# Kernel tuning notes

Measured on AMD Instinct MI355X. Metric: run time of the kernel, lower is better.

## Reference

```python
import jax, jax.numpy as jnp
import numpy as np

N, E, ND, ED, H1, H2 = 50000, 800000, 128, 16, 256, 32
NEG_SLOPE = 0.2


def setup_inputs() -> dict:
    key = jax.random.key(0)
    ks = jax.random.split(key, 12)
    s = lambda k, shape: jax.random.normal(k, shape, jnp.float32) * 0.05
    return dict(
        x=jax.random.normal(ks[0], (N, ND), jnp.float32),
        edge_index=jax.random.randint(ks[1], (2, E), 0, N),
        edge_attr=jax.random.normal(ks[2], (E, ED), jnp.float32),
        Wl1=s(ks[3], (H1, ND)), bl1=jnp.zeros((H1,), jnp.float32),
        Wr1=s(ks[4], (H1, ND)), br1=jnp.zeros((H1,), jnp.float32),
        We1=s(ks[5], (H1, ED)), att1=s(ks[6], (H1,)), bias1=jnp.zeros((H1,), jnp.float32),
        Wl2=s(ks[7], (H2, H1)), bl2=jnp.zeros((H2,), jnp.float32),
        Wr2=s(ks[8], (H2, H1)), br2=jnp.zeros((H2,), jnp.float32),
        We2=s(ks[9], (H2, ED)), att2=s(ks[10], (H2,)), bias2=jnp.zeros((H2,), jnp.float32),
    )


def _gatv2_layer(x, src, dst, ea, Wl, bl, Wr, br, We, att, bias, n):
    # heads=1, concat=True  (PyG GATv2Conv defaults)
    xl = x @ Wl.T + bl                      # [n, C]  source transform
    xr = x @ Wr.T + br                      # [n, C]  target transform
    # per-edge message: x_j + x_i + lin_edge(edge_attr), then LeakyReLU
    m = jax.nn.leaky_relu(xl[src] + xr[dst] + ea @ We.T, NEG_SLOPE)  # [Etot, C]
    logit = m @ att                         # [Etot]
    # segment softmax over destination nodes (numerically stable)
    lmax = jax.ops.segment_max(logit, dst, num_segments=n)
    lmax = jnp.where(jnp.isfinite(lmax), lmax, 0.0)
    a = jnp.exp(logit - lmax[dst])
    denom = jax.ops.segment_sum(a, dst, num_segments=n)
    a = a / denom[dst]                      # self-loops guarantee denom > 0
    # scatter-add of alpha-weighted source features, plus output bias
    return jax.ops.segment_sum(xl[src] * a[:, None], dst, num_segments=n) + bias


def reference(x, edge_index, edge_attr,
              Wl1, bl1, Wr1, br1, We1, att1, bias1,
              Wl2, bl2, Wr2, br2, We2, att2, bias2):
    n = x.shape[0]
    src, dst = edge_index[0], edge_index[1]
    # add_self_loops=True with fill_value='mean': loop attr = mean incoming edge_attr
    deg = jax.ops.segment_sum(jnp.ones_like(dst, jnp.float32), dst, num_segments=n)
    loop_attr = jax.ops.segment_sum(edge_attr, dst, num_segments=n) / jnp.maximum(deg, 1.0)[:, None]
    loop = jnp.arange(n)
    src_f = jnp.concatenate([src, loop])
    dst_f = jnp.concatenate([dst, loop])
    ea = jnp.concatenate([edge_attr, loop_attr], axis=0)
    h = _gatv2_layer(x, src_f, dst_f, ea, Wl1, bl1, Wr1, br1, We1, att1, bias1, n)
    h = _gatv2_layer(h, src_f, dst_f, ea, Wl2, bl2, Wr2, br2, We2, att2, bias2, n)
    return h.mean(axis=0)  # [out_dim]
```

## Files before the change

kernel.cpp:

```cpp
#include <hip/hip_runtime.h>
#include <math.h>

#define N_NODES 50000
#define N_EDGES 800000
#define ND 128
#define ED 16
#define H1 256
#define H2 32
#define NEG_SLOPE 0.2f

typedef _Float16 half2v __attribute__((ext_vector_type(2)));

#if defined(__has_builtin)
#if __has_builtin(__builtin_amdgcn_fdot2)
#define FDOT2(a, b, c) __builtin_amdgcn_fdot2((a), (b), (c), false)
#endif
#endif
#ifndef FDOT2
#define FDOT2(a, b, c) ((float)(a).x * (float)(b).x + (float)(a).y * (float)(b).y + (c))
#endif

__global__ void k_deg(const int* __restrict__ ei, int* __restrict__ counts, int E) {
    int e = blockIdx.x * blockDim.x + threadIdx.x;
    if (e < E) atomicAdd(&counts[ei[E + e]], 1);
}

__global__ void k_scan1(const int* __restrict__ counts, int* __restrict__ partial, int n, int chunk) {
    __shared__ int sh[256];
    int beg = blockIdx.x * chunk, end = min(beg + chunk, n);
    int sum = 0;
    for (int i = beg + threadIdx.x; i < end; i += 256) sum += counts[i] + 1;
    sh[threadIdx.x] = sum;
    __syncthreads();
    for (int off = 128; off; off >>= 1) {
        if (threadIdx.x < off) sh[threadIdx.x] += sh[threadIdx.x + off];
        __syncthreads();
    }
    if (threadIdx.x == 0) partial[blockIdx.x] = sh[0];
}
__global__ void k_scan2(int* __restrict__ partial) {
    __shared__ int sh[256];
    int v = partial[threadIdx.x];
    sh[threadIdx.x] = v;
    __syncthreads();
    for (int off = 1; off < 256; off <<= 1) {
        int t = (threadIdx.x >= off) ? sh[threadIdx.x - off] : 0;
        __syncthreads();
        sh[threadIdx.x] += t;
        __syncthreads();
    }
    partial[threadIdx.x] = sh[threadIdx.x] - v;
}
__global__ void k_scan3(const int* __restrict__ counts, const int* __restrict__ partial,
                        int* __restrict__ rowptr, int n, int chunk) {
    __shared__ int sh[256];
    int beg = blockIdx.x * chunk, end = min(beg + chunk, n);
    int run = partial[blockIdx.x];
    for (int base = beg; base < end; base += 256) {
        int i = base + threadIdx.x;
        int v = (i < end) ? counts[i] + 1 : 0;
        sh[threadIdx.x] = v;
        __syncthreads();
        for (int off = 1; off < 256; off <<= 1) {
            int t = (threadIdx.x >= off) ? sh[threadIdx.x - off] : 0;
            __syncthreads();
            sh[threadIdx.x] += t;
            __syncthreads();
        }
        if (i < end) rowptr[i + 1] = run + sh[threadIdx.x];
        __syncthreads();
        run += sh[255];
        __syncthreads();
    }
    if (blockIdx.x == 0 && threadIdx.x == 0) rowptr[0] = 0;
}

__global__ void k_fill_csr(const int* __restrict__ ei, const float* __restrict__ ea,
                           const int* __restrict__ rowptr, int* __restrict__ fill,
                           int* __restrict__ csr_src, _Float16* __restrict__ ea_h, int E, int n) {
    int idx = blockIdx.x * blockDim.x + threadIdx.x;
    if (idx < E) {
        int dst = ei[E + idx];
        int slot = rowptr[dst] + atomicAdd(&fill[dst], 1);
        csr_src[slot] = ei[idx];
        const float* srow = ea + (size_t)idx * ED;
        _Float16* drow = ea_h + (size_t)slot * ED;
        #pragma unroll
        for (int q = 0; q < 4; ++q) {
            float4 f = ((const float4*)srow)[q];
            drow[q * 4 + 0] = (_Float16)f.x;
            drow[q * 4 + 1] = (_Float16)f.y;
            drow[q * 4 + 2] = (_Float16)f.z;
            drow[q * 4 + 3] = (_Float16)f.w;
        }
    } else if (idx < E + n) {
        int i = idx - E;
        csr_src[rowptr[i + 1] - 1] = i;
    }
}

__global__ void k_loop_mean(_Float16* __restrict__ ea_h, const int* __restrict__ rowptr, int n) {
    int idx = blockIdx.x * blockDim.x + threadIdx.x;
    if (idx >= n * ED) return;
    int node = idx >> 4, d = idx & 15;
    int beg = rowptr[node], last = rowptr[node + 1] - 1;
    float s = 0.f;
    for (int j = beg; j < last; ++j) s += (float)ea_h[(size_t)j * ED + d];
    int cnt = last - beg;
    ea_h[(size_t)last * ED + d] = (_Float16)(s / (float)(cnt > 0 ? cnt : 1));
}

__global__ void k_pack_half(const float* __restrict__ src, _Float16* __restrict__ dst, int total) {
    int i = blockIdx.x * blockDim.x + threadIdx.x;
    if (i < total) dst[i] = (_Float16)src[i];
}

#define GT 64
#define GK 32
#define LDP 68
__global__ __launch_bounds__(256) void k_gemm_dual(const float* __restrict__ X,
                                                   const float* __restrict__ Wa,
                                                   const float* __restrict__ ba,
                                                   float* __restrict__ Ya,
                                                   const float* __restrict__ Wb,
                                                   const float* __restrict__ bb,
                                                   float* __restrict__ Yb,
                                                   int n, int K, int C) {
    __shared__ float xs[GK][LDP];
    __shared__ float ws[GK][LDP];
    int tid = threadIdx.x;
    int tx = tid & 15, ty = tid >> 4;
    int row0 = blockIdx.x * GT, col0 = blockIdx.y * GT;
    float acc[4][4] = {};
    for (int k0 = 0; k0 < K; k0 += GK) {
        #pragma unroll
        for (int l = 0; l < 2; ++l) {
            int t = l * 256 + tid;
            int r = t >> 3, c4 = t & 7;
            int gr = row0 + r;
            float4 xv = {0.f, 0.f, 0.f, 0.f};
            if (gr < n) xv = *(const float4*)(X + (size_t)gr * K + k0 + c4 * 4);
            xs[c4 * 4 + 0][r] = xv.x; xs[c4 * 4 + 1][r] = xv.y;
            xs[c4 * 4 + 2][r] = xv.z; xs[c4 * 4 + 3][r] = xv.w;
            int gc = col0 + r;
            const float* wrow = (gc < C) ? Wa + (size_t)gc * K : Wb + (size_t)(gc - C) * K;
            float4 wv = *(const float4*)(wrow + k0 + c4 * 4);
            ws[c4 * 4 + 0][r] = wv.x; ws[c4 * 4 + 1][r] = wv.y;
            ws[c4 * 4 + 2][r] = wv.z; ws[c4 * 4 + 3][r] = wv.w;
        }
        __syncthreads();
        #pragma unroll
        for (int kk = 0; kk < GK; ++kk) {
            float4 a = *(const float4*)&xs[kk][ty * 4];
            float4 b = *(const float4*)&ws[kk][tx * 4];
            const float* af = (const float*)&a;
            const float* bf = (const float*)&b;
            #pragma unroll
            for (int i = 0; i < 4; ++i)
                #pragma unroll
                for (int j = 0; j < 4; ++j) acc[i][j] += af[i] * bf[j];
        }
        __syncthreads();
    }
    #pragma unroll
    for (int i = 0; i < 4; ++i) {
        int r = row0 + ty * 4 + i;
        if (r >= n) continue;
        #pragma unroll
        for (int j = 0; j < 4; ++j) {
            int c = col0 + tx * 4 + j;
            if (c < C) Ya[(size_t)r * C + c] = acc[i][j] + ba[c];
            else       Yb[(size_t)r * C + (c - C)] = acc[i][j] + bb[c - C];
        }
    }
}

__global__ __launch_bounds__(256) void k_gat1(const float* __restrict__ xl,
                                              const float* __restrict__ xr,
                                              const _Float16* __restrict__ ea_h,
                                              const _Float16* __restrict__ We_h,
                                              const float* __restrict__ att,
                                              const float* __restrict__ bias,
                                              const int* __restrict__ rowptr,
                                              const int* __restrict__ csr_src,
                                              float* __restrict__ out, int n) {
    int lane = threadIdx.x & 63;
    int wave = (blockIdx.x * blockDim.x + threadIdx.x) >> 6;
    int nwaves = (gridDim.x * blockDim.x) >> 6;
    const half2v* Wp = (const half2v*)We_h;
    half2v w[4][8];
    #pragma unroll
    for (int r = 0; r < 4; ++r)
        #pragma unroll
        for (int q = 0; q < 8; ++q) w[r][q] = Wp[(lane * 4 + r) * 8 + q];
    float4 attv = ((const float4*)att)[lane];
    float4 bv = ((const float4*)bias)[lane];

    for (int node = wave; node < n; node += nwaves) {
        float4 xrv = *(const float4*)(xr + (size_t)node * H1 + lane * 4);
        int beg = rowptr[node], end = rowptr[node + 1];
        float denom = 0.f;
        float4 acc = {0.f, 0.f, 0.f, 0.f};
        int j = beg;
        for (; j + 1 < end; j += 2) {
            int sA = csr_src[j], sB = csr_src[j + 1];
            const half2v* eA = (const half2v*)(ea_h + (size_t)j * ED);
            const half2v* eB = (const half2v*)(ea_h + (size_t)(j + 1) * ED);
            half2v a0 = eA[0], a1 = eA[1], a2 = eA[2], a3 = eA[3];
            half2v a4 = eA[4], a5 = eA[5], a6 = eA[6], a7 = eA[7];
            half2v b0 = eB[0], b1 = eB[1], b2 = eB[2], b3 = eB[3];
            half2v b4 = eB[4], b5 = eB[5], b6 = eB[6], b7 = eB[7];
            float4 xlA = *(const float4*)(xl + (size_t)sA * H1 + lane * 4);
            float4 xlB = *(const float4*)(xl + (size_t)sB * H1 + lane * 4);
            float pA = 0.f, pB = 0.f;
            #pragma unroll
            for (int r = 0; r < 4; ++r) {
                float weA = 0.f, weB = 0.f;
                weA = FDOT2(w[r][0], a0, weA); weB = FDOT2(w[r][0], b0, weB);
                weA = FDOT2(w[r][1], a1, weA); weB = FDOT2(w[r][1], b1, weB);
                weA = FDOT2(w[r][2], a2, weA); weB = FDOT2(w[r][2], b2, weB);
                weA = FDOT2(w[r][3], a3, weA); weB = FDOT2(w[r][3], b3, weB);
                weA = FDOT2(w[r][4], a4, weA); weB = FDOT2(w[r][4], b4, weB);
                weA = FDOT2(w[r][5], a5, weA); weB = FDOT2(w[r][5], b5, weB);
                weA = FDOT2(w[r][6], a6, weA); weB = FDOT2(w[r][6], b6, weB);
                weA = FDOT2(w[r][7], a7, weA); weB = FDOT2(w[r][7], b7, weB);
                float tA = ((const float*)&xlA)[r] + ((const float*)&xrv)[r] + weA;
                float tB = ((const float*)&xlB)[r] + ((const float*)&xrv)[r] + weB;
                tA = (tA > 0.f) ? tA : NEG_SLOPE * tA;
                tB = (tB > 0.f) ? tB : NEG_SLOPE * tB;
                pA += ((const float*)&attv)[r] * tA;
                pB += ((const float*)&attv)[r] * tB;
            }
            #pragma unroll
            for (int off = 32; off >= 1; off >>= 1) {
                pA += __shfl_xor(pA, off);
                pB += __shfl_xor(pB, off);
            }
            float peA = __expf(pA), peB = __expf(pB);
            denom += peA + peB;
            acc.x += peA * xlA.x + peB * xlB.x;
            acc.y += peA * xlA.y + peB * xlB.y;
            acc.z += peA * xlA.z + peB * xlB.z;
            acc.w += peA * xlA.w + peB * xlB.w;
        }
        if (j < end) {
            int sA = csr_src[j];
            const half2v* eA = (const half2v*)(ea_h + (size_t)j * ED);
            half2v a0 = eA[0], a1 = eA[1], a2 = eA[2], a3 = eA[3];
            half2v a4 = eA[4], a5 = eA[5], a6 = eA[6], a7 = eA[7];
            float4 xlA = *(const float4*)(xl + (size_t)sA * H1 + lane * 4);
            float pA = 0.f;
            #pragma unroll
            for (int r = 0; r < 4; ++r) {
                float weA = 0.f;
                weA = FDOT2(w[r][0], a0, weA);
                weA = FDOT2(w[r][1], a1, weA);
                weA = FDOT2(w[r][2], a2, weA);
                weA = FDOT2(w[r][3], a3, weA);
                weA = FDOT2(w[r][4], a4, weA);
                weA = FDOT2(w[r][5], a5, weA);
                weA = FDOT2(w[r][6], a6, weA);
                weA = FDOT2(w[r][7], a7, weA);
                float tA = ((const float*)&xlA)[r] + ((const float*)&xrv)[r] + weA;
                tA = (tA > 0.f) ? tA : NEG_SLOPE * tA;
                pA += ((const float*)&attv)[r] * tA;
            }
            #pragma unroll
            for (int off = 32; off >= 1; off >>= 1) pA += __shfl_xor(pA, off);
            float peA = __expf(pA);
            denom += peA;
            acc.x += peA * xlA.x; acc.y += peA * xlA.y;
            acc.z += peA * xlA.z; acc.w += peA * xlA.w;
        }
        float inv = 1.f / denom;
        float4 o;
        o.x = acc.x * inv + bv.x; o.y = acc.y * inv + bv.y;
        o.z = acc.z * inv + bv.z; o.w = acc.w * inv + bv.w;
        *(float4*)(out + (size_t)node * H1 + lane * 4) = o;
    }
}

__global__ __launch_bounds__(256) void k_gat2(const float* __restrict__ xl,
                                              const float* __restrict__ xr,
                                              const _Float16* __restrict__ ea_h,
                                              const _Float16* __restrict__ We_h,
                                              const float* __restrict__ att,
                                              const float* __restrict__ bias,
                                              const int* __restrict__ rowptr,
                                              const int* __restrict__ csr_src,
                                              float* __restrict__ out, int n) {
    int tid = threadIdx.x;
    int c = tid & 31;
    int grp = (blockIdx.x * blockDim.x + tid) >> 5;
    int ngrp = (gridDim.x * blockDim.x) >> 5;
    const half2v* Wp = (const half2v*)We_h;
    half2v w0 = Wp[c * 8 + 0], w1 = Wp[c * 8 + 1], w2 = Wp[c * 8 + 2], w3 = Wp[c * 8 + 3];
    half2v w4 = Wp[c * 8 + 4], w5 = Wp[c * 8 + 5], w6 = Wp[c * 8 + 6], w7 = Wp[c * 8 + 7];
    float attc = att[c], bc = bias[c];

    for (int node = grp; node < n; node += ngrp) {
        float xrc = xr[(size_t)node * H2 + c];
        int beg = rowptr[node], end = rowptr[node + 1];
        float denom = 0.f, acc = 0.f;
        int j = beg;
        for (; j + 1 < end; j += 2) {
            int sA = csr_src[j], sB = csr_src[j + 1];
            const half2v* eA = (const half2v*)(ea_h + (size_t)j * ED);
            const half2v* eB = (const half2v*)(ea_h + (size_t)(j + 1) * ED);
            half2v a0 = eA[0], a1 = eA[1], a2 = eA[2], a3 = eA[3];
            half2v a4 = eA[4], a5 = eA[5], a6 = eA[6], a7 = eA[7];
            half2v b0 = eB[0], b1 = eB[1], b2 = eB[2], b3 = eB[3];
            half2v b4 = eB[4], b5 = eB[5], b6 = eB[6], b7 = eB[7];
            float xlA = xl[(size_t)sA * H2 + c];
            float xlB = xl[(size_t)sB * H2 + c];
            float weA = 0.f, weB = 0.f;
            weA = FDOT2(w0, a0, weA); weB = FDOT2(w0, b0, weB);
            weA = FDOT2(w1, a1, weA); weB = FDOT2(w1, b1, weB);
            weA = FDOT2(w2, a2, weA); weB = FDOT2(w2, b2, weB);
            weA = FDOT2(w3, a3, weA); weB = FDOT2(w3, b3, weB);
            weA = FDOT2(w4, a4, weA); weB = FDOT2(w4, b4, weB);
            weA = FDOT2(w5, a5, weA); weB = FDOT2(w5, b5, weB);
            weA = FDOT2(w6, a6, weA); weB = FDOT2(w6, b6, weB);
            weA = FDOT2(w7, a7, weA); weB = FDOT2(w7, b7, weB);
            float tA = xlA + xrc + weA;
            float tB = xlB + xrc + weB;
            tA = (tA > 0.f) ? tA : NEG_SLOPE * tA;
            tB = (tB > 0.f) ? tB : NEG_SLOPE * tB;
            float pA = attc * tA, pB = attc * tB;
            #pragma unroll
            for (int off = 16; off >= 1; off >>= 1) {
                pA += __shfl_xor(pA, off);
                pB += __shfl_xor(pB, off);
            }
            float peA = __expf(pA), peB = __expf(pB);
            denom += peA + peB;
            acc += peA * xlA + peB * xlB;
        }
        if (j < end) {
            int sA = csr_src[j];
            const half2v* eA = (const half2v*)(ea_h + (size_t)j * ED);
            half2v a0 = eA[0], a1 = eA[1], a2 = eA[2], a3 = eA[3];
            half2v a4 = eA[4], a5 = eA[5], a6 = eA[6], a7 = eA[7];
            float xlA = xl[(size_t)sA * H2 + c];
            float weA = 0.f;
            weA = FDOT2(w0, a0, weA);
            weA = FDOT2(w1, a1, weA);
            weA = FDOT2(w2, a2, weA);
            weA = FDOT2(w3, a3, weA);
            weA = FDOT2(w4, a4, weA);
            weA = FDOT2(w5, a5, weA);
            weA = FDOT2(w6, a6, weA);
            weA = FDOT2(w7, a7, weA);
            float tA = xlA + xrc + weA;
            tA = (tA > 0.f) ? tA : NEG_SLOPE * tA;
            float pA = attc * tA;
            #pragma unroll
            for (int off = 16; off >= 1; off >>= 1) pA += __shfl_xor(pA, off);
            float peA = __expf(pA);
            denom += peA;
            acc += peA * xlA;
        }
        out[(size_t)node * H2 + c] = acc / denom + bc;
    }
}

__global__ __launch_bounds__(256) void k_mean(const float* __restrict__ h2,
                                              float* __restrict__ out, int total, float invN) {
    __shared__ float red[H2];
    int tid = threadIdx.x;
    if (tid < H2) red[tid] = 0.f;
    __syncthreads();
    float part = 0.f;
    for (int idx = blockIdx.x * blockDim.x + tid; idx < total; idx += gridDim.x * blockDim.x)
        part += h2[idx];
    atomicAdd(&red[tid & 31], part);
    __syncthreads();
    if (tid < H2) atomicAdd(&out[tid], red[tid] * invN);
}

extern "C" void kernel_launch(void* const* d_in, const int* in_sizes, int n_in,
                              void* d_out, int out_size, void* d_ws, size_t ws_size,
                              hipStream_t stream) {
    const float* x   = (const float*)d_in[0];
    const int*   ei  = (const int*)d_in[1];
    const float* ea  = (const float*)d_in[2];
    const float* Wl1 = (const float*)d_in[3];
    const float* bl1 = (const float*)d_in[4];
    const float* Wr1 = (const float*)d_in[5];
    const float* br1 = (const float*)d_in[6];
    const float* We1 = (const float*)d_in[7];
    const float* at1 = (const float*)d_in[8];
    const float* bi1 = (const float*)d_in[9];
    const float* Wl2 = (const float*)d_in[10];
    const float* bl2 = (const float*)d_in[11];
    const float* Wr2 = (const float*)d_in[12];
    const float* br2 = (const float*)d_in[13];
    const float* We2 = (const float*)d_in[14];
    const float* at2 = (const float*)d_in[15];
    const float* bi2 = (const float*)d_in[16];
    float* out = (float*)d_out;

    const int N = N_NODES, E = N_EDGES, ET = N_EDGES + N_NODES;
    const int SCAN_CHUNK = (N + 255) / 256;

    size_t off = 0;
    auto carve = [&](size_t bytes) {
        void* p = (char*)d_ws + off;
        off += (bytes + 255) & ~(size_t)255;
        return p;
    };
    int*      counts  = (int*)carve((size_t)N * 4);
    int*      fill    = (int*)carve((size_t)N * 4);
    int*      rowptr  = (int*)carve((size_t)(N + 1) * 4);
    int*      partial = (int*)carve(256 * 4);
    int*      csr_src = (int*)carve((size_t)ET * 4);
    _Float16* ea_h    = (_Float16*)carve((size_t)ET * ED * 2);
    _Float16* We1_h   = (_Float16*)carve((size_t)H1 * ED * 2);
    _Float16* We2_h   = (_Float16*)carve((size_t)H2 * ED * 2);
    float*    xl1     = (float*)carve((size_t)N * H1 * 4);
    float*    xr1     = (float*)carve((size_t)N * H1 * 4);
    float*    h1      = (float*)carve((size_t)N * H1 * 4);
    float* xl2 = xr1;
    float* xr2 = xr1 + (size_t)N * H2;
    float* h2  = xr1 + 2 * (size_t)N * H2;

    hipMemsetAsync(counts, 0, (size_t)N * 4, stream);
    hipMemsetAsync(fill, 0, (size_t)N * 4, stream);
    hipMemsetAsync(out, 0, (size_t)H2 * 4, stream);

    k_deg<<<(E + 255) / 256, 256, 0, stream>>>(ei, counts, E);
    k_scan1<<<256, 256, 0, stream>>>(counts, partial, N, SCAN_CHUNK);
    k_scan2<<<1, 256, 0, stream>>>(partial);
    k_scan3<<<256, 256, 0, stream>>>(counts, partial, rowptr, N, SCAN_CHUNK);
    k_fill_csr<<<(E + N + 255) / 256, 256, 0, stream>>>(ei, ea, rowptr, fill, csr_src, ea_h, E, N);
    k_loop_mean<<<(N * ED + 255) / 256, 256, 0, stream>>>(ea_h, rowptr, N);
    k_pack_half<<<(H1 * ED + 255) / 256, 256, 0, stream>>>(We1, We1_h, H1 * ED);
    k_pack_half<<<(H2 * ED + 255) / 256, 256, 0, stream>>>(We2, We2_h, H2 * ED);

    k_gemm_dual<<<dim3((N + GT - 1) / GT, (2 * H1) / GT), 256, 0, stream>>>(
        x, Wl1, bl1, xl1, Wr1, br1, xr1, N, ND, H1);
    k_gat1<<<4096, 256, 0, stream>>>(xl1, xr1, ea_h, We1_h, at1, bi1,
                                     rowptr, csr_src, h1, N);

    k_gemm_dual<<<dim3((N + GT - 1) / GT, (2 * H2) / GT), 256, 0, stream>>>(
        h1, Wl2, bl2, xl2, Wr2, br2, xr2, N, H1, H2);
    k_gat2<<<2048, 256, 0, stream>>>(xl2, xr2, ea_h, We2_h, at2, bi2,
                                     rowptr, csr_src, h2, N);

    k_mean<<<128, 256, 0, stream>>>(h2, out, N * H2, 1.0f / (float)N);
}
```

Before: 499.9 us.

## Use bf16 MFMA GEMMs, fp16 gather features, and restructure GAT kernels

Replaces the fp32 shared-memory GEMM with a bf16 MFMA GEMM that reads pre-packed bf16 inputs and concatenated weights. Layer-1 source features are stored in fp16 and consumed with mixed-precision FMA, which halves gather traffic. Layer-1 output is written as bf16, and the LeakyReLU-attention product is rewritten algebraically using abs. The layer-2 GAT kernel now handles two edges per wave with wave-level node assignment. The lower precision adds rounding error to intermediate activations, and extra pack kernels add launches.

```diff
diff --git a/kernel.cpp b/kernel.cpp
--- a/kernel.cpp
+++ b/kernel.cpp
@@ -7,18 +7,28 @@
 #define ED 16
 #define H1 256
 #define H2 32
-#define NEG_SLOPE 0.2f
-
-typedef _Float16 half2v __attribute__((ext_vector_type(2)));
-
-#if defined(__has_builtin)
-#if __has_builtin(__builtin_amdgcn_fdot2)
-#define FDOT2(a, b, c) __builtin_amdgcn_fdot2((a), (b), (c), false)
-#endif
-#endif
-#ifndef FDOT2
-#define FDOT2(a, b, c) ((float)(a).x * (float)(b).x + (float)(a).y * (float)(b).y + (c))
-#endif
+
+typedef short bf16x8 __attribute__((ext_vector_type(8)));
+typedef float f32x4 __attribute__((ext_vector_type(4)));
+
+__device__ __forceinline__ float dot2h(uint a, uint b, float c) {
+    asm("v_dot2_f32_f16 %0, %1, %2, %0" : "+v"(c) : "v"(a), "v"(b));
+    return c;
+}
+__device__ __forceinline__ float fmamix_lo(uint a, float b, float c) {
+    float d;
+    asm("v_fma_mix_f32 %0, %1, %2, %3 op_sel_hi:[1,0,0]" : "=v"(d) : "v"(a), "v"(b), "v"(c));
+    return d;
+}
+__device__ __forceinline__ float fmamix_hi(uint a, float b, float c) {
+    float d;
+    asm("v_fma_mix_f32 %0, %1, %2, %3 op_sel:[1,0,0] op_sel_hi:[1,0,0]" : "=v"(d) : "v"(a), "v"(b), "v"(c));
+    return d;
+}
+__device__ __forceinline__ ushort f2bf(float f) {
+    uint u = __float_as_uint(f);
+    return (ushort)((u + 0x7fff + ((u >> 16) & 1)) >> 16);
+}
 
 __global__ void k_deg(const int* __restrict__ ei, int* __restrict__ counts, int E) {
     int e = blockIdx.x * blockDim.x + threadIdx.x;
@@ -114,68 +124,70 @@
     int i = blockIdx.x * blockDim.x + threadIdx.x;
     if (i < total) dst[i] = (_Float16)src[i];
 }
-
-#define GT 64
-#define GK 32
-#define LDP 68
-__global__ __launch_bounds__(256) void k_gemm_dual(const float* __restrict__ X,
-                                                   const float* __restrict__ Wa,
+__global__ void k_pack_bf16x4(const float* __restrict__ src, ushort* __restrict__ dst, int total4) {
+    int i = blockIdx.x * blockDim.x + threadIdx.x;
+    if (i >= total4) return;
+    float4 f = ((const float4*)src)[i];
+    ushort4 o;
+    o.x = f2bf(f.x); o.y = f2bf(f.y); o.z = f2bf(f.z); o.w = f2bf(f.w);
+    ((ushort4*)dst)[i] = o;
+}
+__global__ void k_pack_wcat(const float* __restrict__ Wa, const float* __restrict__ Wb,
+                            ushort* __restrict__ dst, int C, int K) {
+    int i = blockIdx.x * blockDim.x + threadIdx.x;
+    if (i >= 2 * C * K) return;
+    int row = i / K, k = i - row * K;
+    float v = (row < C) ? Wa[(size_t)row * K + k] : Wb[(size_t)(row - C) * K + k];
+    dst[i] = f2bf(v);
+}
+
+template <int HALF_A>
+__global__ __launch_bounds__(256) void k_gemm_mfma(const ushort* __restrict__ Xb,
+                                                   const ushort* __restrict__ Wc,
                                                    const float* __restrict__ ba,
-                                                   float* __restrict__ Ya,
-                                                   const float* __restrict__ Wb,
                                                    const float* __restrict__ bb,
+                                                   void* __restrict__ Ya,
                                                    float* __restrict__ Yb,
                                                    int n, int K, int C) {
-    __shared__ float xs[GK][LDP];
-    __shared__ float ws[GK][LDP];
     int tid = threadIdx.x;
-    int tx = tid & 15, ty = tid >> 4;
-    int row0 = blockIdx.x * GT, col0 = blockIdx.y * GT;
-    float acc[4][4] = {};
-    for (int k0 = 0; k0 < K; k0 += GK) {
+    int lane = tid & 63, wv = tid >> 6;
+    int r = lane & 15, kg = lane >> 4;
+    int row0 = blockIdx.x * 64 + wv * 16;
+    int colblk = blockIdx.y * 64;
+    int arow = row0 + r;
+    if (arow >= n) arow = n - 1;
+    const ushort* aptr = Xb + (size_t)arow * K + kg * 8;
+    f32x4 acc[4] = {};
+    for (int k0 = 0; k0 < K; k0 += 32) {
+        bf16x8 av = *(const bf16x8*)(aptr + k0);
         #pragma unroll
-        for (int l = 0; l < 2; ++l) {
-            int t = l * 256 + tid;
-            int r = t >> 3, c4 = t & 7;
-            int gr = row0 + r;
-            float4 xv = {0.f, 0.f, 0.f, 0.f};
-            if (gr < n) xv = *(const float4*)(X + (size_t)gr * K + k0 + c4 * 4);
-            xs[c4 * 4 + 0][r] = xv.x; xs[c4 * 4 + 1][r] = xv.y;
-            xs[c4 * 4 + 2][r] = xv.z; xs[c4 * 4 + 3][r] = xv.w;
-            int gc = col0 + r;
-            const float* wrow = (gc < C) ? Wa + (size_t)gc * K : Wb + (size_t)(gc - C) * K;
-            float4 wv = *(const float4*)(wrow + k0 + c4 * 4);
-            ws[c4 * 4 + 0][r] = wv.x; ws[c4 * 4 + 1][r] = wv.y;
-            ws[c4 * 4 + 2][r] = wv.z; ws[c4 * 4 + 3][r] = wv.w;
-        }
-        __syncthreads();
+        for (int t = 0; t < 4; ++t) {
+            const ushort* bptr = Wc + (size_t)(colblk + t * 16 + r) * K + k0 + kg * 8;
+            bf16x8 bv = *(const bf16x8*)bptr;
+            acc[t] = __builtin_amdgcn_mfma_f32_16x16x32_bf16(av, bv, acc[t], 0, 0, 0);
+        }
+    }
+    #pragma unroll
+    for (int t = 0; t < 4; ++t) {
+        int col = colblk + t * 16 + r;
+        int rowb = row0 + kg * 4;
         #pragma unroll
-        for (int kk = 0; kk < GK; ++kk) {
-            float4 a = *(const float4*)&xs[kk][ty * 4];
-            float4 b = *(const float4*)&ws[kk][tx * 4];
-            const float* af = (const float*)&a;
-            const float* bf = (const float*)&b;
-            #pragma unroll
-            for (int i = 0; i < 4; ++i)
-                #pragma unroll
-                for (int j = 0; j < 4; ++j) acc[i][j] += af[i] * bf[j];
-        }
-        __syncthreads();
-    }
-    #pragma unroll
-    for (int i = 0; i < 4; ++i) {
-        int r = row0 + ty * 4 + i;
-        if (r >= n) continue;
-        #pragma unroll
-        for (int j = 0; j < 4; ++j) {
-            int c = col0 + tx * 4 + j;
-            if (c < C) Ya[(size_t)r * C + c] = acc[i][j] + ba[c];
-            else       Yb[(size_t)r * C + (c - C)] = acc[i][j] + bb[c - C];
-        }
-    }
-}
-
-__global__ __launch_bounds__(256) void k_gat1(const float* __restrict__ xl,
+        for (int q = 0; q < 4; ++q) {
+            int row = rowb + q;
+            if (row >= n) continue;
+            float v = acc[t][q];
+            if (col < C) {
+                v += ba[col];
+                if (HALF_A) ((_Float16*)Ya)[(size_t)row * C + col] = (_Float16)v;
+                else        ((float*)Ya)[(size_t)row * C + col] = v;
+            } else {
+                Yb[(size_t)row * C + (col - C)] = v + bb[col - C];
+            }
+        }
+    }
+}
+
+__global__ __launch_bounds__(256) void k_gat1(const _Float16* __restrict__ xlh,
                                               const float* __restrict__ xr,
                                               const _Float16* __restrict__ ea_h,
                                               const _Float16* __restrict__ We_h,
@@ -183,54 +195,70 @@
                                               const float* __restrict__ bias,
                                               const int* __restrict__ rowptr,
                                               const int* __restrict__ csr_src,
-                                              float* __restrict__ out, int n) {
-    int lane = threadIdx.x & 63;
+                                              ushort* __restrict__ out_bf, int n) {
+    const int lane = threadIdx.x & 63;
     int wave = (blockIdx.x * blockDim.x + threadIdx.x) >> 6;
     int nwaves = (gridDim.x * blockDim.x) >> 6;
-    const half2v* Wp = (const half2v*)We_h;
-    half2v w[4][8];
+    const uint* Wp = (const uint*)We_h;
+    uint w0[8], w1[8], w2[8], w3[8];
     #pragma unroll
-    for (int r = 0; r < 4; ++r)
-        #pragma unroll
-        for (int q = 0; q < 8; ++q) w[r][q] = Wp[(lane * 4 + r) * 8 + q];
+    for (int q = 0; q < 8; ++q) {
+        w0[q] = Wp[(lane * 4 + 0) * 8 + q];
+        w1[q] = Wp[(lane * 4 + 1) * 8 + q];
+        w2[q] = Wp[(lane * 4 + 2) * 8 + q];
+        w3[q] = Wp[(lane * 4 + 3) * 8 + q];
+    }
     float4 attv = ((const float4*)att)[lane];
     float4 bv = ((const float4*)bias)[lane];
+    float a06x = 0.6f * attv.x, a06y = 0.6f * attv.y, a06z = 0.6f * attv.z, a06w = 0.6f * attv.w;
+    float a04x = 0.4f * attv.x, a04y = 0.4f * attv.y, a04z = 0.4f * attv.z, a04w = 0.4f * attv.w;
+    const float fone = 1.0f;
+    const uint laneoff = (uint)lane << 3;
 
     for (int node = wave; node < n; node += nwaves) {
-        float4 xrv = *(const float4*)(xr + (size_t)node * H1 + lane * 4);
+        float4 xrv = *(const float4*)(xr + ((size_t)node << 8) + (lane << 2));
         int beg = rowptr[node], end = rowptr[node + 1];
-        float denom = 0.f;
-        float4 acc = {0.f, 0.f, 0.f, 0.f};
+        float denom = 0.f, ac0 = 0.f, ac1 = 0.f, ac2 = 0.f, ac3 = 0.f;
         int j = beg;
         for (; j + 1 < end; j += 2) {
-            int sA = csr_src[j], sB = csr_src[j + 1];
-            const half2v* eA = (const half2v*)(ea_h + (size_t)j * ED);
-            const half2v* eB = (const half2v*)(ea_h + (size_t)(j + 1) * ED);
-            half2v a0 = eA[0], a1 = eA[1], a2 = eA[2], a3 = eA[3];
-            half2v a4 = eA[4], a5 = eA[5], a6 = eA[6], a7 = eA[7];
-            half2v b0 = eB[0], b1 = eB[1], b2 = eB[2], b3 = eB[3];
-            half2v b4 = eB[4], b5 = eB[5], b6 = eB[6], b7 = eB[7];
-            float4 xlA = *(const float4*)(xl + (size_t)sA * H1 + lane * 4);
-            float4 xlB = *(const float4*)(xl + (size_t)sB * H1 + lane * 4);
-            float pA = 0.f, pB = 0.f;
-            #pragma unroll
-            for (int r = 0; r < 4; ++r) {
-                float weA = 0.f, weB = 0.f;
-                weA = FDOT2(w[r][0], a0, weA); weB = FDOT2(w[r][0], b0, weB);
-                weA = FDOT2(w[r][1], a1, weA); weB = FDOT2(w[r][1], b1, weB);
-                weA = FDOT2(w[r][2], a2, weA); weB = FDOT2(w[r][2], b2, weB);
-                weA = FDOT2(w[r][3], a3, weA); weB = FDOT2(w[r][3], b3, weB);
-                weA = FDOT2(w[r][4], a4, weA); weB = FDOT2(w[r][4], b4, weB);
-                weA = FDOT2(w[r][5], a5, weA); weB = FDOT2(w[r][5], b5, weB);
-                weA = FDOT2(w[r][6], a6, weA); weB = FDOT2(w[r][6], b6, weB);
-                weA = FDOT2(w[r][7], a7, weA); weB = FDOT2(w[r][7], b7, weB);
-                float tA = ((const float*)&xlA)[r] + ((const float*)&xrv)[r] + weA;
-                float tB = ((const float*)&xlB)[r] + ((const float*)&xrv)[r] + weB;
-                tA = (tA > 0.f) ? tA : NEG_SLOPE * tA;
-                tB = (tB > 0.f) ? tB : NEG_SLOPE * tB;
-                pA += ((const float*)&attv)[r] * tA;
-                pB += ((const float*)&attv)[r] * tB;
-            }
+            int sA = __builtin_amdgcn_readfirstlane(csr_src[j]);
+            int sB = __builtin_amdgcn_readfirstlane(csr_src[j + 1]);
+            const uint4* eP = (const uint4*)((const char*)ea_h + ((uint)j << 5));
+            uint4 eA0 = eP[0], eA1 = eP[1], eB0 = eP[2], eB1 = eP[3];
+            uint2 xA = *(const uint2*)((const char*)xlh + (((uint)sA << 9) + laneoff));
+            uint2 xB = *(const uint2*)((const char*)xlh + (((uint)sB << 9) + laneoff));
+            float weA0 = dot2h(w0[7], eA1.w, dot2h(w0[6], eA1.z, dot2h(w0[5], eA1.y, dot2h(w0[4], eA1.x,
+                         dot2h(w0[3], eA0.w, dot2h(w0[2], eA0.z, dot2h(w0[1], eA0.y, dot2h(w0[0], eA0.x, 0.f))))))));
+            float weA1 = dot2h(w1[7], eA1.w, dot2h(w1[6], eA1.z, dot2h(w1[5], eA1.y, dot2h(w1[4], eA1.x,
+                         dot2h(w1[3], eA0.w, dot2h(w1[2], eA0.z, dot2h(w1[1], eA0.y, dot2h(w1[0], eA0.x, 0.f))))))));
+            float weA2 = dot2h(w2[7], eA1.w, dot2h(w2[6], eA1.z, dot2h(w2[5], eA1.y, dot2h(w2[4], eA1.x,
+                         dot2h(w2[3], eA0.w, dot2h(w2[2], eA0.z, dot2h(w2[1], eA0.y, dot2h(w2[0], eA0.x, 0.f))))))));
+            float weA3 = dot2h(w3[7], eA1.w, dot2h(w3[6], eA1.z, dot2h(w3[5], eA1.y, dot2h(w3[4], eA1.x,
+                         dot2h(w3[3], eA0.w, dot2h(w3[2], eA0.z, dot2h(w3[1], eA0.y, dot2h(w3[0], eA0.x, 0.f))))))));
+            float weB0 = dot2h(w0[7], eB1.w, dot2h(w0[6], eB1.z, dot2h(w0[5], eB1.y, dot2h(w0[4], eB1.x,
+                         dot2h(w0[3], eB0.w, dot2h(w0[2], eB0.z, dot2h(w0[1], eB0.y, dot2h(w0[0], eB0.x, 0.f))))))));
+            float weB1 = dot2h(w1[7], eB1.w, dot2h(w1[6], eB1.z, dot2h(w1[5], eB1.y, dot2h(w1[4], eB1.x,
+                         dot2h(w1[3], eB0.w, dot2h(w1[2], eB0.z, dot2h(w1[1], eB0.y, dot2h(w1[0], eB0.x, 0.f))))))));
+            float weB2 = dot2h(w2[7], eB1.w, dot2h(w2[6], eB1.z, dot2h(w2[5], eB1.y, dot2h(w2[4], eB1.x,
+                         dot2h(w2[3], eB0.w, dot2h(w2[2], eB0.z, dot2h(w2[1], eB0.y, dot2h(w2[0], eB0.x, 0.f))))))));
+            float weB3 = dot2h(w3[7], eB1.w, dot2h(w3[6], eB1.z, dot2h(w3[5], eB1.y, dot2h(w3[4], eB1.x,
+                         dot2h(w3[3], eB0.w, dot2h(w3[2], eB0.z, dot2h(w3[1], eB0.y, dot2h(w3[0], eB0.x, 0.f))))))));
+            float zA0 = fmamix_lo(xA.x, fone, weA0 + xrv.x);
+            float zA1 = fmamix_hi(xA.x, fone, weA1 + xrv.y);
+            float zA2 = fmamix_lo(xA.y, fone, weA2 + xrv.z);
+            float zA3 = fmamix_hi(xA.y, fone, weA3 + xrv.w);
+            float zB0 = fmamix_lo(xB.x, fone, weB0 + xrv.x);
+            float zB1 = fmamix_hi(xB.x, fone, weB1 + xrv.y);
+            float zB2 = fmamix_lo(xB.y, fone, weB2 + xrv.z);
+            float zB3 = fmamix_hi(xB.y, fone, weB3 + xrv.w);
+            float pA = fmaf(a06x, zA0, fmaf(a04x, fabsf(zA0),
+                       fmaf(a06y, zA1, fmaf(a04y, fabsf(zA1),
+                       fmaf(a06z, zA2, fmaf(a04z, fabsf(zA2),
+                       fmaf(a06w, zA3, a04w * fabsf(zA3))))))));
+            float pB = fmaf(a06x, zB0, fmaf(a04x, fabsf(zB0),
+                       fmaf(a06y, zB1, fmaf(a04y, fabsf(zB1),
+                       fmaf(a06z, zB2, fmaf(a04z, fabsf(zB2),
+                       fmaf(a06w, zB3, a04w * fabsf(zB3))))))));
             #pragma unroll
             for (int off = 32; off >= 1; off >>= 1) {
                 pA += __shfl_xor(pA, off);
@@ -238,45 +266,48 @@
             }
             float peA = __expf(pA), peB = __expf(pB);
             denom += peA + peB;
-            acc.x += peA * xlA.x + peB * xlB.x;
-            acc.y += peA * xlA.y + peB * xlB.y;
-            acc.z += peA * xlA.z + peB * xlB.z;
-            acc.w += peA * xlA.w + peB * xlB.w;
+            ac0 = fmamix_lo(xB.x, peB, fmamix_lo(xA.x, peA, ac0));
+            ac1 = fmamix_hi(xB.x, peB, fmamix_hi(xA.x, peA, ac1));
+            ac2 = fmamix_lo(xB.y, peB, fmamix_lo(xA.y, peA, ac2));
+            ac3 = fmamix_hi(xB.y, peB, fmamix_hi(xA.y, peA, ac3));
         }
         if (j < end) {
-            int sA = csr_src[j];
-            const half2v* eA = (const half2v*)(ea_h + (size_t)j * ED);
-            half2v a0 = eA[0], a1 = eA[1], a2 = eA[2], a3 = eA[3];
-            half2v a4 = eA[4], a5 = eA[5], a6 = eA[6], a7 = eA[7];
-            float4 xlA = *(const float4*)(xl + (size_t)sA * H1 + lane * 4);
-            float pA = 0.f;
-            #pragma unroll
-            for (int r = 0; r < 4; ++r) {
-                float weA = 0.f;
-                weA = FDOT2(w[r][0], a0, weA);
-                weA = FDOT2(w[r][1], a1, weA);
-                weA = FDOT2(w[r][2], a2, weA);
-                weA = FDOT2(w[r][3], a3, weA);
-                weA = FDOT2(w[r][4], a4, weA);
-                weA = FDOT2(w[r][5], a5, weA);
-                weA = FDOT2(w[r][6], a6, weA);
-                weA = FDOT2(w[r][7], a7, weA);
-                float tA = ((const float*)&xlA)[r] + ((const float*)&xrv)[r] + weA;
-                tA = (tA > 0.f) ? tA : NEG_SLOPE * tA;
-                pA += ((const float*)&attv)[r] * tA;
-            }
+            int sA = __builtin_amdgcn_readfirstlane(csr_src[j]);
+            const uint4* eP = (const uint4*)((const char*)ea_h + ((uint)j << 5));
+            uint4 eA0 = eP[0], eA1 = eP[1];
+            uint2 xA = *(const uint2*)((const char*)xlh + (((uint)sA << 9) + laneoff));
+            float weA0 = dot2h(w0[7], eA1.w, dot2h(w0[6], eA1.z, dot2h(w0[5], eA1.y, dot2h(w0[4], eA1.x,
+                         dot2h(w0[3], eA0.w, dot2h(w0[2], eA0.z, dot2h(w0[1], eA0.y, dot2h(w0[0], eA0.x, 0.f))))))));
+            float weA1 = dot2h(w1[7], eA1.w, dot2h(w1[6], eA1.z, dot2h(w1[5], eA1.y, dot2h(w1[4], eA1.x,
+                         dot2h(w1[3], eA0.w, dot2h(w1[2], eA0.z, dot2h(w1[1], eA0.y, dot2h(w1[0], eA0.x, 0.f))))))));
+            float weA2 = dot2h(w2[7], eA1.w, dot2h(w2[6], eA1.z, dot2h(w2[5], eA1.y, dot2h(w2[4], eA1.x,
+                         dot2h(w2[3], eA0.w, dot2h(w2[2], eA0.z, dot2h(w2[1], eA0.y, dot2h(w2[0], eA0.x, 0.f))))))));
+            float weA3 = dot2h(w3[7], eA1.w, dot2h(w3[6], eA1.z, dot2h(w3[5], eA1.y, dot2h(w3[4], eA1.x,
+                         dot2h(w3[3], eA0.w, dot2h(w3[2], eA0.z, dot2h(w3[1], eA0.y, dot2h(w3[0], eA0.x, 0.f))))))));
+            float zA0 = fmamix_lo(xA.x, fone, weA0 + xrv.x);
+            float zA1 = fmamix_hi(xA.x, fone, weA1 + xrv.y);
+            float zA2 = fmamix_lo(xA.y, fone, weA2 + xrv.z);
+            float zA3 = fmamix_hi(xA.y, fone, weA3 + xrv.w);
+            float pA = fmaf(a06x, zA0, fmaf(a04x, fabsf(zA0),
+                       fmaf(a06y, zA1, fmaf(a04y, fabsf(zA1),
+                       fmaf(a06z, zA2, fmaf(a04z, fabsf(zA2),
+                       fmaf(a06w, zA3, a04w * fabsf(zA3))))))));
             #pragma unroll
             for (int off = 32; off >= 1; off >>= 1) pA += __shfl_xor(pA, off);
             float peA = __expf(pA);
             denom += peA;
-            acc.x += peA * xlA.x; acc.y += peA * xlA.y;
-            acc.z += peA * xlA.z; acc.w += peA * xlA.w;
+            ac0 = fmamix_lo(xA.x, peA, ac0);
+            ac1 = fmamix_hi(xA.x, peA, ac1);
+            ac2 = fmamix_lo(xA.y, peA, ac2);
+            ac3 = fmamix_hi(xA.y, peA, ac3);
         }
         float inv = 1.f / denom;
-        float4 o;
-        o.x = acc.x * inv + bv.x; o.y = acc.y * inv + bv.y;
-        o.z = acc.z * inv + bv.z; o.w = acc.w * inv + bv.w;
-        *(float4*)(out + (size_t)node * H1 + lane * 4) = o;
+        ushort4 o;
+        o.x = f2bf(fmaf(ac0, inv, bv.x));
+        o.y = f2bf(fmaf(ac1, inv, bv.y));
+        o.z = f2bf(fmaf(ac2, inv, bv.z));
+        o.w = f2bf(fmaf(ac3, inv, bv.w));
+        *(ushort4*)(out_bf + ((size_t)node << 8) + (lane << 2)) = o;
     }
 }
 
@@ -290,77 +321,42 @@
                                               const int* __restrict__ csr_src,
                                               float* __restrict__ out, int n) {
     int tid = threadIdx.x;
-    int c = tid & 31;
-    int grp = (blockIdx.x * blockDim.x + tid) >> 5;
-    int ngrp = (gridDim.x * blockDim.x) >> 5;
-    const half2v* Wp = (const half2v*)We_h;
-    half2v w0 = Wp[c * 8 + 0], w1 = Wp[c * 8 + 1], w2 = Wp[c * 8 + 2], w3 = Wp[c * 8 + 3];
-    half2v w4 = Wp[c * 8 + 4], w5 = Wp[c * 8 + 5], w6 = Wp[c * 8 + 6], w7 = Wp[c * 8 + 7];
-    float attc = att[c], bc = bias[c];
-
-    for (int node = grp; node < n; node += ngrp) {
-        float xrc = xr[(size_t)node * H2 + c];
+    int lane = tid & 63;
+    int sub = lane >> 5, c = lane & 31;
+    int wave = (blockIdx.x * blockDim.x + tid) >> 6;
+    int nwaves = (gridDim.x * blockDim.x) >> 6;
+    const uint* Wp = (const uint*)We_h;
+    uint w0 = Wp[c * 8 + 0], w1 = Wp[c * 8 + 1], w2 = Wp[c * 8 + 2], w3 = Wp[c * 8 + 3];
+    uint w4 = Wp[c * 8 + 4], w5 = Wp[c * 8 + 5], w6 = Wp[c * 8 + 6], w7 = Wp[c * 8 + 7];
+    float attc = att[c];
+    float a06 = 0.6f * attc, a04 = 0.4f * attc;
+    float bc = bias[c];
+
+    for (int node = wave; node < n; node += nwaves) {
+        float xrc = xr[((size_t)node << 5) + c];
         int beg = rowptr[node], end = rowptr[node + 1];
         float denom = 0.f, acc = 0.f;
-        int j = beg;
-        for (; j + 1 < end; j += 2) {
-            int sA = csr_src[j], sB = csr_src[j + 1];
-            const half2v* eA = (const half2v*)(ea_h + (size_t)j * ED);
-            const half2v* eB = (const half2v*)(ea_h + (size_t)(j + 1) * ED);
-            half2v a0 = eA[0], a1 = eA[1], a2 = eA[2], a3 = eA[3];
-            half2v a4 = eA[4], a5 = eA[5], a6 = eA[6], a7 = eA[7];
-            half2v b0 = eB[0], b1 = eB[1], b2 = eB[2], b3 = eB[3];
-            half2v b4 = eB[4], b5 = eB[5], b6 = eB[6], b7 = eB[7];
-            float xlA = xl[(size_t)sA * H2 + c];
-            float xlB = xl[(size_t)sB * H2 + c];
-            float weA = 0.f, weB = 0.f;
-            weA = FDOT2(w0, a0, weA); weB = FDOT2(w0, b0, weB);
-            weA = FDOT2(w1, a1, weA); weB = FDOT2(w1, b1, weB);
-            weA = FDOT2(w2, a2, weA); weB = FDOT2(w2, b2, weB);
-            weA = FDOT2(w3, a3, weA); weB = FDOT2(w3, b3, weB);
-            weA = FDOT2(w4, a4, weA); weB = FDOT2(w4, b4, weB);
-            weA = FDOT2(w5, a5, weA); weB = FDOT2(w5, b5, weB);
-            weA = FDOT2(w6, a6, weA); weB = FDOT2(w6, b6, weB);
-            weA = FDOT2(w7, a7, weA); weB = FDOT2(w7, b7, weB);
-            float tA = xlA + xrc + weA;
-            float tB = xlB + xrc + weB;
-            tA = (tA > 0.f) ? tA : NEG_SLOPE * tA;
-            tB = (tB > 0.f) ? tB : NEG_SLOPE * tB;
-            float pA = attc * tA, pB = attc * tB;
+        for (int j = beg; j < end; j += 2) {
+            int jj = j + sub;
+            bool act = jj < end;
+            int js = act ? jj : j;
+            int s = csr_src[js];
+            const uint4* eP = (const uint4*)((const char*)ea_h + ((uint)js << 5));
+            uint4 e0 = eP[0], e1 = eP[1];
+            float xlv = *(const float*)((const char*)xl + (((uint)s << 7) + (c << 2)));
+            float we = dot2h(w7, e1.w, dot2h(w6, e1.z, dot2h(w5, e1.y, dot2h(w4, e1.x,
+                       dot2h(w3, e0.w, dot2h(w2, e0.z, dot2h(w1, e0.y, dot2h(w0, e0.x, 0.f))))))));
+            float z = xlv + xrc + we;
+            float p = fmaf(a06, z, a04 * fabsf(z));
             #pragma unroll
-            for (int off = 16; off >= 1; off >>= 1) {
-                pA += __shfl_xor(pA, off);
-                pB += __shfl_xor(pB, off);
-            }
-            float peA = __expf(pA), peB = __expf(pB);
-            denom += peA + peB;
-            acc += peA * xlA + peB * xlB;
-        }
-        if (j < end) {
-            int sA = csr_src[j];
-            const half2v* eA = (const half2v*)(ea_h + (size_t)j * ED);
-            half2v a0 = eA[0], a1 = eA[1], a2 = eA[2], a3 = eA[3];
-            half2v a4 = eA[4], a5 = eA[5], a6 = eA[6], a7 = eA[7];
-            float xlA = xl[(size_t)sA * H2 + c];
-            float weA = 0.f;
-            weA = FDOT2(w0, a0, weA);
-            weA = FDOT2(w1, a1, weA);
-            weA = FDOT2(w2, a2, weA);
-            weA = FDOT2(w3, a3, weA);
-            weA = FDOT2(w4, a4, weA);
-            weA = FDOT2(w5, a5, weA);
-            weA = FDOT2(w6, a6, weA);
-            weA = FDOT2(w7, a7, weA);
-            float tA = xlA + xrc + weA;
-            tA = (tA > 0.f) ? tA : NEG_SLOPE * tA;
-            float pA = attc * tA;
-            #pragma unroll
-            for (int off = 16; off >= 1; off >>= 1) pA += __shfl_xor(pA, off);
-            float peA = __expf(pA);
-            denom += peA;
-            acc += peA * xlA;
-        }
-        out[(size_t)node * H2 + c] = acc / denom + bc;
+            for (int off = 16; off >= 1; off >>= 1) p += __shfl_xor(p, off);
+            float pe = act ? __expf(p) : 0.f;
+            denom += pe;
+            acc = fmaf(pe, xlv, acc);
+        }
+        acc += __shfl_xor(acc, 32);
+        denom += __shfl_xor(denom, 32);
+        if (sub == 0) out[((size_t)node << 5) + c] = acc / denom + bc;
     }
 }
 
@@ -417,12 +413,15 @@
     _Float16* ea_h    = (_Float16*)carve((size_t)ET * ED * 2);
     _Float16* We1_h   = (_Float16*)carve((size_t)H1 * ED * 2);
     _Float16* We2_h   = (_Float16*)carve((size_t)H2 * ED * 2);
-    float*    xl1     = (float*)carve((size_t)N * H1 * 4);
+    ushort*   x_bf    = (ushort*)carve((size_t)N * ND * 2);
+    ushort*   wcat1   = (ushort*)carve((size_t)2 * H1 * ND * 2);
+    ushort*   wcat2   = (ushort*)carve((size_t)2 * H2 * H1 * 2);
+    _Float16* xl1h    = (_Float16*)carve((size_t)N * H1 * 2);
     float*    xr1     = (float*)carve((size_t)N * H1 * 4);
-    float*    h1      = (float*)carve((size_t)N * H1 * 4);
-    float* xl2 = xr1;
-    float* xr2 = xr1 + (size_t)N * H2;
-    float* h2  = xr1 + 2 * (size_t)N * H2;
+    ushort*   h1_bf   = (ushort*)carve((size_t)N * H1 * 2);
+    float*    xl2     = (float*)carve((size_t)N * H2 * 4);
+    float*    xr2     = (float*)carve((size_t)N * H2 * 4);
+    float*    h2      = (float*)carve((size_t)N * H2 * 4);
 
     hipMemsetAsync(counts, 0, (size_t)N * 4, stream);
     hipMemsetAsync(fill, 0, (size_t)N * 4, stream);
@@ -436,16 +435,19 @@
     k_loop_mean<<<(N * ED + 255) / 256, 256, 0, stream>>>(ea_h, rowptr, N);
     k_pack_half<<<(H1 * ED + 255) / 256, 256, 0, stream>>>(We1, We1_h, H1 * ED);
     k_pack_half<<<(H2 * ED + 255) / 256, 256, 0, stream>>>(We2, We2_h, H2 * ED);
-
-    k_gemm_dual<<<dim3((N + GT - 1) / GT, (2 * H1) / GT), 256, 0, stream>>>(
-        x, Wl1, bl1, xl1, Wr1, br1, xr1, N, ND, H1);
-    k_gat1<<<4096, 256, 0, stream>>>(xl1, xr1, ea_h, We1_h, at1, bi1,
-                                     rowptr, csr_src, h1, N);
-
-    k_gemm_dual<<<dim3((N + GT - 1) / GT, (2 * H2) / GT), 256, 0, stream>>>(
-        h1, Wl2, bl2, xl2, Wr2, br2, xr2, N, H1, H2);
-    k_gat2<<<2048, 256, 0, stream>>>(xl2, xr2, ea_h, We2_h, at2, bi2,
-                                     rowptr, csr_src, h2, N);
+    k_pack_bf16x4<<<(N * ND / 4 + 255) / 256, 256, 0, stream>>>(x, x_bf, N * ND / 4);
+    k_pack_wcat<<<(2 * H1 * ND + 255) / 256, 256, 0, stream>>>(Wl1, Wr1, wcat1, H1, ND);
+    k_pack_wcat<<<(2 * H2 * H1 + 255) / 256, 256, 0, stream>>>(Wl2, Wr2, wcat2, H2, H1);
+
+    k_gemm_mfma<1><<<dim3((N + 63) / 64, (2 * H1) / 64), 256, 0, stream>>>(
+        x_bf, wcat1, bl1, br1, (void*)xl1h, xr1, N, ND, H1);
+    k_gat1<<<4096, 256, 0, stream>>>(xl1h, xr1, ea_h, We1_h, at1, bi1,
+                                     rowptr, csr_src, h1_bf, N);
+
+    k_gemm_mfma<0><<<dim3((N + 63) / 64, (2 * H2) / 64), 256, 0, stream>>>(
+        h1_bf, wcat2, bl2, br2, (void*)xl2, xr2, N, H1, H2);
+    k_gat2<<<12500, 256, 0, stream>>>(xl2, xr2, ea_h, We2_h, at2, bi2,
+                                      rowptr, csr_src, h2, N);
 
     k_mean<<<128, 256, 0, stream>>>(h2, out, N * H2, 1.0f / (float)N);
 }
```

Result: no change. 501.0 us (+0.2%).
